# Kernel tuning notes

Hardware: AMD Instinct MI355X
Metric: run time of the kernel (lower is better)

The kernel has to match this reference:

```python
import jax, jax.numpy as jnp
import numpy as np

D = 1024      # d_model
HD = 128      # shared k/v head dim == attn_expert_dim
EA = 8        # attention experts
KA = 2        # attention top-k
EF = 16       # ffn experts
KF = 2        # ffn top-k
FH = 512      # ffn expert hidden dim
MAXP = 64     # max relative positions
B, S = 4, 1024
EPS = 1e-5


def setup_inputs() -> dict:
    key = jax.random.key(0)
    ks = jax.random.split(key, 12)
    r = lambda i, shape, scale=0.02: jax.random.normal(ks[i], shape, jnp.float32) * scale
    return {
        "src": jax.random.normal(ks[0], (B, S, D), jnp.float32),
        "ln1_w": jnp.ones((D,), jnp.float32), "ln1_b": jnp.zeros((D,), jnp.float32),
        "ln2_w": jnp.ones((D,), jnp.float32), "ln2_b": jnp.zeros((D,), jnp.float32),
        "attn_gate_w": r(1, (D, EA)),
        "q_w": r(2, (EA, D, HD)), "q_b": jnp.zeros((EA, HD), jnp.float32),
        "k_w": r(3, (D, HD)), "k_b": jnp.zeros((HD,), jnp.float32),
        "v_w": r(4, (D, HD)), "v_b": jnp.zeros((HD,), jnp.float32),
        "o_w": r(5, (EA, HD, D)), "o_b": jnp.zeros((EA, D), jnp.float32),
        "rel_table": r(6, (2 * MAXP + 1, HD)),
        "ff_gate_w": r(7, (D, EF)),
        "ff_w1": r(8, (EF, D, FH)), "ff_b1": jnp.zeros((EF, FH), jnp.float32),
        "ff_w2": r(9, (EF, FH, D)), "ff_b2": jnp.zeros((EF, D), jnp.float32),
    }


def _layer_norm(x, w, b):
    mu = x.mean(-1, keepdims=True)
    var = ((x - mu) ** 2).mean(-1, keepdims=True)
    return (x - mu) * jax.lax.rsqrt(var + EPS) * w + b


def _topk_gates(logits, k):
    # top-k over router logits, softmax over the selected k, scatter to dense [.., E]
    top_vals, top_idx = jax.lax.top_k(logits, k)
    g = jax.nn.softmax(top_vals, axis=-1)
    onehot = jax.nn.one_hot(top_idx, logits.shape[-1], dtype=logits.dtype)  # [...,k,E]
    return jnp.einsum('...k,...ke->...e', g, onehot)


def _moa(x, gate_w, q_w, q_b, k_w, k_b, v_w, v_b, o_w, o_b, rel_table):
    # Mixture-of-attention: per-expert q/out projections, shared k/v, Shaw rel-pos.
    S_ = x.shape[1]
    gates = _topk_gates(x @ gate_w, KA)                                  # [B,S,EA]
    q = (jnp.einsum('bsd,edh->bseh', x, q_w) + q_b) * (HD ** -0.5)       # [B,S,EA,HD]
    k = x @ k_w + k_b                                                    # [B,S,HD]
    v = x @ v_w + v_b
    scores = jnp.einsum('bqeh,bkh->beqk', q, k)                          # [B,EA,S,S]
    rel_s = jnp.einsum('bqeh,rh->beqr', q, rel_table)                    # [B,EA,S,R]
    pos = jnp.arange(S_)
    rel_idx = jnp.clip(pos[None, :] - pos[:, None], -MAXP, MAXP) + MAXP  # [S,S]
    scores = scores + jnp.take_along_axis(rel_s, rel_idx[None, None], axis=-1)
    p = jax.nn.softmax(scores, axis=-1)
    ctx = jnp.einsum('beqk,bkh->bqeh', p, v)                             # [B,S,EA,HD]
    out = jnp.einsum('bqeh,ehd,bqe->bqd', ctx, o_w, gates)
    return out + jnp.einsum('bqe,ed->bqd', gates, o_b)


def _moe_ffn(x, gate_w, w1, b1, w2, b2):
    gates = _topk_gates(x @ gate_w, KF)                                  # [B,S,EF]
    h = jax.nn.relu(jnp.einsum('bsd,edh->bseh', x, w1) + b1)             # [B,S,EF,FH]
    out = jnp.einsum('bseh,ehd,bse->bsd', h, w2, gates)
    return out + jnp.einsum('bse,ed->bsd', gates, b2)


def reference(src, ln1_w, ln1_b, ln2_w, ln2_b, attn_gate_w, q_w, q_b, k_w, k_b,
              v_w, v_b, o_w, o_b, rel_table, ff_gate_w, ff_w1, ff_b1, ff_w2, ff_b2):
    # pre-LN residual block around MoE attention
    res = src
    xn = _layer_norm(src, ln1_w, ln1_b)
    x = res + _moa(xn, attn_gate_w, q_w, q_b, k_w, k_b, v_w, v_b, o_w, o_b, rel_table)
    # pre-LN residual block around MoE FFN
    res = x
    xn = _layer_norm(x, ln2_w, ln2_b)
    return res + _moe_ffn(xn, ff_gate_w, ff_w1, ff_b1, ff_w2, ff_b2)
```

## Files before the change

kernel.cpp:

```cpp
#include <hip/hip_runtime.h>

#define D 1024
#define HD 128
#define EA 8
#define EF 16
#define FH 512
#define MAXPOS 64
#define RNUM 129
#define RSTRIDE 132
#define SEQ 1024
#define NTOK 4096
#define NPAIR (NTOK * 2)
#define NPAD 8320
#define LN_EPS 1e-5f
#define QSCALE 0.08838834764831845f
#define BSTR 32
#define PROW 2048
#define NSPL 2

typedef __attribute__((ext_vector_type(8))) short bf16x8;
typedef __attribute__((ext_vector_type(4))) float f32x4;
typedef __attribute__((ext_vector_type(8))) unsigned short u16x8;

__device__ inline ushort f2b(float f) {
    union { float f; unsigned u; } v; v.f = f;
    unsigned r = (v.u + 0x7fffu + ((v.u >> 16) & 1u)) >> 16;
    return (ushort)r;
}
__device__ inline float b2f(ushort u) {
    union { unsigned u; float f; } v; v.u = (unsigned)u << 16; return v.f;
}

__device__ __forceinline__ void gll(const void* g, void* l) {
    __builtin_amdgcn_global_load_lds((const __attribute__((address_space(1))) void*)g,
                                     (__attribute__((address_space(3))) void*)l, 16, 0, 0);
}
__device__ __forceinline__ void wait_vm0() { asm volatile("s_waitcnt vmcnt(0)" ::: "memory"); }
__device__ __forceinline__ void wait_vm3() { asm volatile("s_waitcnt vmcnt(3)" ::: "memory"); }
__device__ __forceinline__ void bar() { __builtin_amdgcn_s_barrier(); }

__device__ inline void mfma_step(const short* Asb, const short* Bsb,
                                 int wr, int wc, int m16, int q, f32x4 (&acc)[2][4]) {
    bf16x8 af[2], bfr[4];
#pragma unroll
    for (int i = 0; i < 2; i++) af[i] = *(const bf16x8*)&Asb[(wr + i * 16 + m16) * BSTR + q * 8];
#pragma unroll
    for (int j = 0; j < 4; j++) bfr[j] = *(const bf16x8*)&Bsb[(wc + j * 16 + m16) * BSTR + q * 8];
#pragma unroll
    for (int i = 0; i < 2; i++)
#pragma unroll
        for (int j = 0; j < 4; j++)
            acc[i][j] = __builtin_amdgcn_mfma_f32_16x16x32_bf16(af[i], bfr[j], acc[i][j], 0, 0, 0);
}

#define KLOOP(NK, AP, BP0, BP1, STRIDE)                                          \
    gll(AP, &As[0][w * 512]); gll(BP0, &Bs[0][w * 1024]); gll(BP1, &Bs[0][w * 1024 + 512]); \
    gll(AP + STRIDE, &As[1][w * 512]); gll(BP0 + STRIDE, &Bs[1][w * 1024]);      \
    gll(BP1 + STRIDE, &Bs[1][w * 1024 + 512]);                                   \
    {                                                                            \
        int cur = 0;                                                             \
        for (int k = 0; k < NK; k++) {                                           \
            if (k < NK - 1) wait_vm3(); else wait_vm0();                         \
            bar();                                                               \
            mfma_step(As[cur], Bs[cur], wr, wc, m16, q, acc);                    \
            if (k + 2 < NK) {                                                    \
                bar();                                                           \
                gll(AP + (k + 2) * STRIDE, &As[cur][w * 512]);                   \
                gll(BP0 + (k + 2) * STRIDE, &Bs[cur][w * 1024]);                 \
                gll(BP1 + (k + 2) * STRIDE, &Bs[cur][w * 1024 + 512]);           \
            }                                                                    \
            cur ^= 1;                                                            \
        }                                                                        \
    }

__global__ void ln_kernel(const float* __restrict__ x, const float* __restrict__ w,
                          const float* __restrict__ b, float* __restrict__ y,
                          ushort* __restrict__ yb) {
    int row = blockIdx.x;
    const float* xr = x + (size_t)row * D;
    float v[4];
    float s = 0.f, s2 = 0.f;
#pragma unroll
    for (int i = 0; i < 4; i++) {
        v[i] = xr[threadIdx.x + i * 256];
        s += v[i]; s2 += v[i] * v[i];
    }
#pragma unroll
    for (int off = 32; off; off >>= 1) { s += __shfl_down(s, off); s2 += __shfl_down(s2, off); }
    __shared__ float red0[4], red1[4];
    int wave = threadIdx.x >> 6, lane = threadIdx.x & 63;
    if (lane == 0) { red0[wave] = s; red1[wave] = s2; }
    __syncthreads();
    float ts = red0[0] + red0[1] + red0[2] + red0[3];
    float ts2 = red1[0] + red1[1] + red1[2] + red1[3];
    float mu = ts * (1.f / D);
    float var = ts2 * (1.f / D) - mu * mu;
    float inv = rsqrtf(var + LN_EPS);
#pragma unroll
    for (int i = 0; i < 4; i++) {
        int d = threadIdx.x + i * 256;
        float o = (v[i] - mu) * inv * w[d] + b[d];
        y[(size_t)row * D + d] = o;
        yb[(size_t)row * D + d] = f2b(o);
    }
}

template <int E>
__global__ void router_kernel(const float* __restrict__ xn, const float* __restrict__ gw,
                              int* __restrict__ idx, float* __restrict__ gate) {
    int t = blockIdx.x;
    int lane = threadIdx.x;
    float acc[E];
#pragma unroll
    for (int e = 0; e < E; e++) acc[e] = 0.f;
    const float* xr = xn + (size_t)t * D;
    for (int d = lane; d < D; d += 64) {
        float xv = xr[d];
#pragma unroll
        for (int e = 0; e < E; e++) acc[e] += xv * gw[d * E + e];
    }
#pragma unroll
    for (int e = 0; e < E; e++) {
#pragma unroll
        for (int off = 32; off; off >>= 1) acc[e] += __shfl_down(acc[e], off);
    }
    if (lane == 0) {
        float v0 = -1e30f, v1 = -1e30f;
        int i0 = 0, i1 = 0;
#pragma unroll
        for (int e = 0; e < E; e++) {
            float a = acc[e];
            if (a > v0) { v1 = v0; i1 = i0; v0 = a; i0 = e; }
            else if (a > v1) { v1 = a; i1 = e; }
        }
        float g0 = 1.f / (1.f + expf(v1 - v0));
        idx[t * 2] = i0; idx[t * 2 + 1] = i1;
        gate[t * 2] = g0; gate[t * 2 + 1] = 1.f - g0;
    }
}

__global__ void zero_meta(int* __restrict__ ameta, int* __restrict__ fmeta) {
    if (threadIdx.x < 105) ameta[threadIdx.x] = 0;
    if (threadIdx.x < 48) fmeta[threadIdx.x] = 0;
}

__global__ void abin_count(const int* __restrict__ aidx, int* __restrict__ meta) {
    int i = blockIdx.x * 256 + threadIdx.x;
    if (i < NPAIR) {
        int e = aidx[i];
        int b = (i >> 1) >> 10;
        atomicAdd(&meta[e * 4 + b], 1);
    }
}
__global__ void abin_scan(int* __restrict__ meta) {
    if (threadIdx.x == 0 && blockIdx.x == 0) {
        int s = 0;
        for (int bin = 0; bin < 32; bin++) {
            if ((bin & 3) == 0) meta[96 + (bin >> 2)] = s;
            meta[32 + bin] = s; meta[64 + bin] = s; s += meta[bin];
        }
        meta[96 + 8] = s;
    }
}
__global__ void abin_scatter(const int* __restrict__ aidx, int* __restrict__ meta,
                             int* __restrict__ list, int* __restrict__ inv) {
    int i = blockIdx.x * 256 + threadIdx.x;
    if (i < NPAIR) {
        int e = aidx[i];
        int b = (i >> 1) >> 10;
        int pos = atomicAdd(&meta[64 + e * 4 + b], 1);
        list[pos] = i;
        inv[i] = pos;
    }
}

__global__ void bin_count(const int* __restrict__ fidx, int* __restrict__ meta) {
    int i = blockIdx.x * 256 + threadIdx.x;
    if (i < NPAIR) atomicAdd(&meta[fidx[i]], 1);
}
__global__ void bin_scan(int* __restrict__ meta) {
    if (threadIdx.x == 0 && blockIdx.x == 0) {
        int s = 0;
        for (int e = 0; e < EF; e++) { meta[16 + e] = s; meta[32 + e] = s; s += meta[e]; }
    }
}
__global__ void bin_scatter(const int* __restrict__ fidx, int* __restrict__ meta,
                            int* __restrict__ list, int* __restrict__ inv) {
    int i = blockIdx.x * 256 + threadIdx.x;
    if (i < NPAIR) {
        int e = fidx[i];
        int pos = atomicAdd(&meta[32 + e], 1);
        list[pos] = i;
        inv[i] = pos;
    }
}

template <int R, int C>
__device__ __forceinline__ void convT_body(const float* __restrict__ src, ushort* __restrict__ dst) {
    int r0 = blockIdx.x * 32, c0 = blockIdx.y * 32;
    __shared__ float tile[32][33];
    int tx = threadIdx.x & 31, ty = threadIdx.x >> 5;
#pragma unroll
    for (int i = 0; i < 32; i += 8)
        tile[ty + i][tx] = src[(size_t)(r0 + ty + i) * C + c0 + tx];
    __syncthreads();
#pragma unroll
    for (int i = 0; i < 32; i += 8)
        dst[(size_t)(c0 + ty + i) * R + r0 + tx] = f2b(tile[tx][ty + i]);
}
template <int R, int C>
__global__ void convT_kernel(const float* __restrict__ in, ushort* __restrict__ out) {
    int e = blockIdx.z;
    convT_body<R, C>(in + (size_t)e * R * C, out + (size_t)e * C * R);
}
__global__ void convT_kv(const float* __restrict__ kw, const float* __restrict__ vw,
                         ushort* __restrict__ kwt, ushort* __restrict__ vwt) {
    if (blockIdx.z == 0) convT_body<1024, 128>(kw, kwt);
    else                 convT_body<1024, 128>(vw, vwt);
}

__global__ void conv_kernel(const float* __restrict__ in, ushort* __restrict__ out, int n) {
    int i = blockIdx.x * 256 + threadIdx.x;
    if (i < n) out[i] = f2b(in[i]);
}

__global__ __launch_bounds__(256) void kv_mfma(
    const ushort* __restrict__ xnb, const ushort* __restrict__ kwt,
    const ushort* __restrict__ vwt, float* __restrict__ kpart, float* __restrict__ vpart) {
    const ushort* W = blockIdx.z ? vwt : kwt;
    float* outp = blockIdx.z ? vpart : kpart;
    int m0 = blockIdx.x * 64;
    int s = blockIdx.y;
    int kbase = s * 512;
    __shared__ __align__(16) short As[2][64 * BSTR];
    __shared__ __align__(16) short Bs[2][128 * BSTR];
    int tid = threadIdx.x, w = tid >> 6, lane = tid & 63;
    int sr = lane >> 2, sc = (lane & 3) * 8;
    const ushort* ap = xnb + (size_t)(m0 + w * 16 + sr) * D + kbase + sc;
    const ushort* bp0 = W + (size_t)(w * 32 + sr) * D + kbase + sc;
    const ushort* bp1 = bp0 + (size_t)16 * D;
    int wr = (w >> 1) * 32, wc = (w & 1) * 64;
    int m16 = lane & 15, q = lane >> 4;
    f32x4 acc[2][4] = {};
    KLOOP(16, ap, bp0, bp1, 32)
#pragma unroll
    for (int i = 0; i < 2; i++)
#pragma unroll
        for (int r = 0; r < 4; r++) {
            int m = m0 + wr + i * 16 + q * 4 + r;
#pragma unroll
            for (int j = 0; j < 4; j++)
                outp[((size_t)s * NTOK + m) * HD + wc + j * 16 + m16] = acc[i][j][r];
        }
}

__global__ void kv_reduce(const float* __restrict__ kpart, const float* __restrict__ vpart,
                          const float* __restrict__ kb, const float* __restrict__ vb,
                          ushort* __restrict__ kb16, float* __restrict__ vbf) {
    int t = blockIdx.x, h = threadIdx.x;
    float ka = kb[h], va = vb[h];
#pragma unroll
    for (int s = 0; s < NSPL; s++) {
        ka += kpart[((size_t)s * NTOK + t) * HD + h];
        va += vpart[((size_t)s * NTOK + t) * HD + h];
    }
    kb16[(size_t)t * HD + h] = f2b(ka);
    vbf[(size_t)t * HD + h] = va;
}

__global__ __launch_bounds__(256) void q_mfma(
    const ushort* __restrict__ xnb, const ushort* __restrict__ qwt,
    const int* __restrict__ meta, const int* __restrict__ list, float* __restrict__ qpart) {
    int e = blockIdx.z;
    int o = meta[96 + e], c = meta[97 + e] - o;
    int m0 = blockIdx.x * 64;
    if (m0 >= c) return;
    int s = blockIdx.y;
    int kbase = s * 512;
    __shared__ __align__(16) short As[2][64 * BSTR];
    __shared__ __align__(16) short Bs[2][128 * BSTR];
    int tid = threadIdx.x, w = tid >> 6, lane = tid & 63;
    int sr = lane >> 2, sc = (lane & 3) * 8;
    int ri = o + m0 + w * 16 + sr; if (ri > NPAIR - 1) ri = NPAIR - 1;
    const ushort* ap = xnb + (size_t)(list[ri] >> 1) * D + kbase + sc;
    const ushort* bp0 = qwt + (size_t)e * HD * D + (size_t)(w * 32 + sr) * D + kbase + sc;
    const ushort* bp1 = bp0 + (size_t)16 * D;
    int wr = (w >> 1) * 32, wc = (w & 1) * 64;
    int m16 = lane & 15, q = lane >> 4;
    f32x4 acc[2][4] = {};
    KLOOP(16, ap, bp0, bp1, 32)
#pragma unroll
    for (int i = 0; i < 2; i++)
#pragma unroll
        for (int r = 0; r < 4; r++) {
            int pos = o + m0 + wr + i * 16 + q * 4 + r;
            if (pos < o + c) {
#pragma unroll
                for (int j = 0; j < 4; j++)
                    qpart[((size_t)s * NPAD + pos) * HD + wc + j * 16 + m16] = acc[i][j][r];
            }
        }
}

__global__ void q_reduce(const float* __restrict__ qpart, const float* __restrict__ qb,
                         const int* __restrict__ aidx, const int* __restrict__ list,
                         ushort* __restrict__ Qg) {
    int pos = blockIdx.x, h = threadIdx.x;
    int e = aidx[list[pos]];
    float a = qb[e * HD + h];
#pragma unroll
    for (int s = 0; s < NSPL; s++) a += qpart[((size_t)s * NPAD + pos) * HD + h];
    Qg[(size_t)pos * HD + h] = f2b(a * QSCALE);
}

__global__ __launch_bounds__(256) void rel_mfma(
    const ushort* __restrict__ Qg, const ushort* __restrict__ relb,
    float* __restrict__ R) {
    int m0 = blockIdx.x * 64;
    int n0 = blockIdx.y * 128;
    __shared__ __align__(16) short As[2][64 * BSTR];
    __shared__ __align__(16) short Bs[2][128 * BSTR];
    int tid = threadIdx.x, w = tid >> 6, lane = tid & 63;
    int sr = lane >> 2, sc = (lane & 3) * 8;
    const ushort* ap = Qg + (size_t)(m0 + w * 16 + sr) * HD + sc;
    int r0 = n0 + w * 32 + sr;      if (r0 > RNUM - 1) r0 = RNUM - 1;
    int r1 = n0 + w * 32 + 16 + sr; if (r1 > RNUM - 1) r1 = RNUM - 1;
    const ushort* bp0 = relb + (size_t)r0 * HD + sc;
    const ushort* bp1 = relb + (size_t)r1 * HD + sc;
    int wr = (w >> 1) * 32, wc = (w & 1) * 64;
    int m16 = lane & 15, q = lane >> 4;
    f32x4 acc[2][4] = {};
    KLOOP(4, ap, bp0, bp1, 32)
#pragma unroll
    for (int i = 0; i < 2; i++)
#pragma unroll
        for (int r = 0; r < 4; r++) {
            int pos = m0 + wr + i * 16 + q * 4 + r;
#pragma unroll
            for (int j = 0; j < 4; j++) {
                int n = n0 + wc + j * 16 + m16;
                if (n < RNUM) R[(size_t)pos * RSTRIDE + n] = acc[i][j][r];
            }
        }
}

__global__ __launch_bounds__(256) void s_mfma(
    const ushort* __restrict__ Qg, const ushort* __restrict__ kb16,
    const float* __restrict__ R, const int* __restrict__ meta,
    const int* __restrict__ list, float* __restrict__ S) {
    int bin = blockIdx.z;
    int o = meta[32 + bin], c = meta[bin];
    int m0 = blockIdx.x * 64;
    if (m0 >= c) return;
    int b = bin & 3;
    int n0 = blockIdx.y * 128;
    __shared__ __align__(16) short As[2][64 * BSTR];
    __shared__ __align__(16) short Bs[2][128 * BSTR];
    int tid = threadIdx.x, w = tid >> 6, lane = tid & 63;
    int sr = lane >> 2, sc = (lane & 3) * 8;
    int ar = o + m0 + w * 16 + sr; if (ar > NPAIR - 1) ar = NPAIR - 1;
    const ushort* ap = Qg + (size_t)ar * HD + sc;
    const ushort* bp0 = kb16 + ((size_t)b * SEQ + n0 + w * 32 + sr) * HD + sc;
    const ushort* bp1 = bp0 + (size_t)16 * HD;
    int wr = (w >> 1) * 32, wc = (w & 1) * 64;
    int m16 = lane & 15, q = lane >> 4;
    f32x4 acc[2][4] = {};
    KLOOP(4, ap, bp0, bp1, 32)
#pragma unroll
    for (int i = 0; i < 2; i++)
#pragma unroll
        for (int r = 0; r < 4; r++) {
            int pos = o + m0 + wr + i * 16 + q * 4 + r;
            if (pos < o + c) {
                int qpos = (list[pos] >> 1) & (SEQ - 1);
                const float* Rrow = R + (size_t)pos * RSTRIDE;
                float* sr_ = S + (size_t)pos * SEQ;
#pragma unroll
                for (int j = 0; j < 4; j++) {
                    int key = n0 + wc + j * 16 + m16;
                    int rix = key - qpos;
                    rix = (rix < -MAXPOS ? -MAXPOS : (rix > MAXPOS ? MAXPOS : rix)) + MAXPOS;
                    sr_[key] = acc[i][j][r] + Rrow[rix];
                }
            }
        }
}

__global__ __launch_bounds__(256) void softmax_kernel(float* __restrict__ S) {
    int row = blockIdx.x;
    float4* sr = (float4*)(S + (size_t)row * SEQ);
    float4 v = sr[threadIdx.x];
    float m = fmaxf(fmaxf(v.x, v.y), fmaxf(v.z, v.w));
#pragma unroll
    for (int off = 32; off; off >>= 1) m = fmaxf(m, __shfl_down(m, off));
    __shared__ float red0[4], red1[4];
    int wave = threadIdx.x >> 6, lane = threadIdx.x & 63;
    if (lane == 0) red0[wave] = m;
    __syncthreads();
    m = fmaxf(fmaxf(red0[0], red0[1]), fmaxf(red0[2], red0[3]));
    v.x = __expf(v.x - m); v.y = __expf(v.y - m);
    v.z = __expf(v.z - m); v.w = __expf(v.w - m);
    float s = v.x + v.y + v.z + v.w;
#pragma unroll
    for (int off = 32; off; off >>= 1) s += __shfl_down(s, off);
    if (lane == 0) red1[wave] = s;
    __syncthreads();
    float inv = 1.f / (red1[0] + red1[1] + red1[2] + red1[3]);
    ushort* pr = (ushort*)(S + (size_t)row * SEQ);
    ushort4 p4 = { f2b(v.x * inv), f2b(v.y * inv), f2b(v.z * inv), f2b(v.w * inv) };
    *(ushort4*)(pr + threadIdx.x * 4) = p4;
}

__global__ __launch_bounds__(256) void pv_mfma(
    const ushort* __restrict__ Pb, const ushort* __restrict__ vt16,
    const int* __restrict__ meta, float* __restrict__ ppart) {
    int bin = blockIdx.z;
    int o = meta[32 + bin], c = meta[bin];
    int m0 = blockIdx.x * 64;
    if (m0 >= c) return;
    int b = bin & 3;
    int s = blockIdx.y;
    int kbase = s * 512;
    __shared__ __align__(16) short As[2][64 * BSTR];
    __shared__ __align__(16) short Bs[2][128 * BSTR];
    int tid = threadIdx.x, w = tid >> 6, lane = tid & 63;
    int sr = lane >> 2, sc = (lane & 3) * 8;
    int ar = o + m0 + w * 16 + sr; if (ar > NPAIR - 1) ar = NPAIR - 1;
    const ushort* ap = Pb + (size_t)ar * PROW + kbase + sc;
    const ushort* bp0 = vt16 + (size_t)b * HD * SEQ + (size_t)(w * 32 + sr) * SEQ + kbase + sc;
    const ushort* bp1 = bp0 + (size_t)16 * SEQ;
    int wr = (w >> 1) * 32, wc = (w & 1) * 64;
    int m16 = lane & 15, q = lane >> 4;
    f32x4 acc[2][4] = {};
    KLOOP(16, ap, bp0, bp1, 32)
#pragma unroll
    for (int i = 0; i < 2; i++)
#pragma unroll
        for (int r = 0; r < 4; r++) {
            int pos = o + m0 + wr + i * 16 + q * 4 + r;
            if (pos < o + c) {
#pragma unroll
                for (int j = 0; j < 4; j++)
                    ppart[((size_t)s * NPAD + pos) * HD + wc + j * 16 + m16] = acc[i][j][r];
            }
        }
}

__global__ void pv_reduce(const float* __restrict__ ppart, const float* __restrict__ aga,
                          const int* __restrict__ list, ushort* __restrict__ ctx16) {
    int pos = blockIdx.x, h = threadIdx.x;
    float g = aga[list[pos]];
    float a = 0.f;
#pragma unroll
    for (int s = 0; s < NSPL; s++) a += ppart[((size_t)s * NPAD + pos) * HD + h];
    ctx16[(size_t)pos * HD + h] = f2b(a * g);
}

__global__ __launch_bounds__(256) void o_mfma(
    const ushort* __restrict__ ctx16, const ushort* __restrict__ owt,
    const int* __restrict__ meta, ushort* __restrict__ Ofb) {
    int e = blockIdx.z;
    int o = meta[96 + e], c = meta[97 + e] - o;
    int m0 = blockIdx.x * 64;
    if (m0 >= c) return;
    int n0 = blockIdx.y * 128;
    __shared__ __align__(16) short As[2][64 * BSTR];
    __shared__ __align__(16) short Bs[2][128 * BSTR];
    int tid = threadIdx.x, w = tid >> 6, lane = tid & 63;
    int sr = lane >> 2, sc = (lane & 3) * 8;
    int ar = o + m0 + w * 16 + sr; if (ar > NPAIR - 1) ar = NPAIR - 1;
    const ushort* ap = ctx16 + (size_t)ar * HD + sc;
    const ushort* bp0 = owt + (size_t)e * D * HD + (size_t)(n0 + w * 32 + sr) * HD + sc;
    const ushort* bp1 = bp0 + (size_t)16 * HD;
    int wr = (w >> 1) * 32, wc = (w & 1) * 64;
    int m16 = lane & 15, q = lane >> 4;
    f32x4 acc[2][4] = {};
    KLOOP(4, ap, bp0, bp1, 32)
#pragma unroll
    for (int i = 0; i < 2; i++)
#pragma unroll
        for (int r = 0; r < 4; r++) {
            int pos = o + m0 + wr + i * 16 + q * 4 + r;
            if (pos < o + c) {
#pragma unroll
                for (int j = 0; j < 4; j++)
                    Ofb[(size_t)pos * D + n0 + wc + j * 16 + m16] = f2b(acc[i][j][r]);
            }
        }
}

__global__ void attn_combine(const float* __restrict__ src, const float* __restrict__ ob,
                             const int* __restrict__ aidx, const float* __restrict__ aga,
                             const int* __restrict__ ainv, const ushort* __restrict__ Ofb,
                             float* __restrict__ x1) {
    int t = blockIdx.x, tid = threadIdx.x;
    int e0 = aidx[t * 2], e1 = aidx[t * 2 + 1];
    float g0 = aga[t * 2], g1 = aga[t * 2 + 1];
    int p0 = ainv[t * 2], p1 = ainv[t * 2 + 1];
#pragma unroll
    for (int i = 0; i < 4; i++) {
        int d = tid + i * 256;
        x1[(size_t)t * D + d] = src[(size_t)t * D + d]
                              + g0 * ob[e0 * D + d] + g1 * ob[e1 * D + d]
                              + b2f(Ofb[(size_t)p0 * D + d]) + b2f(Ofb[(size_t)p1 * D + d]);
    }
}

__global__ __launch_bounds__(256) void ffn_mfma1(
    const ushort* __restrict__ xnb2, const ushort* __restrict__ w1t,
    const float* __restrict__ b1, const int* __restrict__ meta,
    const int* __restrict__ list, const float* __restrict__ fga,
    ushort* __restrict__ Hb) {
    int e = blockIdx.z;
    int o = meta[16 + e], c = meta[e];
    int m0 = blockIdx.x * 64;
    if (m0 >= c) return;
    int n0 = blockIdx.y * 128;
    __shared__ __align__(16) short As[2][64 * BSTR];
    __shared__ __align__(16) short Bs[2][128 * BSTR];
    int tid = threadIdx.x, w = tid >> 6, lane = tid & 63;
    int sr = lane >> 2, sc = (lane & 3) * 8;
    int ri = o + m0 + w * 16 + sr; if (ri > NPAIR - 1) ri = NPAIR - 1;
    const ushort* ap = xnb2 + (size_t)(list[ri] >> 1) * D + sc;
    const ushort* bp0 = w1t + ((size_t)e * FH + n0 + w * 32 + sr) * D + sc;
    const ushort* bp1 = bp0 + (size_t)16 * D;
    int wr = (w >> 1) * 32, wc = (w & 1) * 64;
    int m16 = lane & 15, q = lane >> 4;
    f32x4 acc[2][4] = {};
    KLOOP(32, ap, bp0, bp1, 32)
#pragma unroll
    for (int i = 0; i < 2; i++)
#pragma unroll
        for (int r = 0; r < 4; r++) {
            int pos = o + m0 + wr + i * 16 + q * 4 + r;
            if (pos < o + c) {
                float g = fga[list[pos]];
#pragma unroll
                for (int j = 0; j < 4; j++) {
                    int n = n0 + wc + j * 16 + m16;
                    Hb[(size_t)pos * FH + n] = f2b(g * fmaxf(acc[i][j][r] + b1[e * FH + n], 0.f));
                }
            }
        }
}

__global__ __launch_bounds__(256) void ffn_mfma2(
    const ushort* __restrict__ Hb, const ushort* __restrict__ w2t,
    const int* __restrict__ meta, ushort* __restrict__ Of2b) {
    int e = blockIdx.z;
    int o = meta[16 + e], c = meta[e];
    int m0 = blockIdx.x * 64;
    if (m0 >= c) return;
    int n0 = blockIdx.y * 128;
    __shared__ __align__(16) short As[2][64 * BSTR];
    __shared__ __align__(16) short Bs[2][128 * BSTR];
    int tid = threadIdx.x, w = tid >> 6, lane = tid & 63;
    int sr = lane >> 2, sc = (lane & 3) * 8;
    int ar = o + m0 + w * 16 + sr; if (ar > NPAIR - 1) ar = NPAIR - 1;
    const ushort* ap = Hb + (size_t)ar * FH + sc;
    const ushort* bp0 = w2t + ((size_t)e * D + n0 + w * 32 + sr) * FH + sc;
    const ushort* bp1 = bp0 + (size_t)16 * FH;
    int wr = (w >> 1) * 32, wc = (w & 1) * 64;
    int m16 = lane & 15, q = lane >> 4;
    f32x4 acc[2][4] = {};
    KLOOP(16, ap, bp0, bp1, 32)
#pragma unroll
    for (int i = 0; i < 2; i++)
#pragma unroll
        for (int r = 0; r < 4; r++) {
            int pos = o + m0 + wr + i * 16 + q * 4 + r;
            if (pos < o + c) {
#pragma unroll
                for (int j = 0; j < 4; j++)
                    Of2b[(size_t)pos * D + n0 + wc + j * 16 + m16] = f2b(acc[i][j][r]);
            }
        }
}

__global__ void ffn_combine(const float* __restrict__ x1, const float* __restrict__ b2,
                            const int* __restrict__ fidx, const float* __restrict__ fga,
                            const int* __restrict__ finv, const ushort* __restrict__ Of2b,
                            float* __restrict__ out) {
    int t = blockIdx.x, tid = threadIdx.x;
    int e0 = fidx[t * 2], e1 = fidx[t * 2 + 1];
    float g0 = fga[t * 2], g1 = fga[t * 2 + 1];
    int p0 = finv[t * 2], p1 = finv[t * 2 + 1];
#pragma unroll
    for (int i = 0; i < 4; i++) {
        int d = tid + i * 256;
        out[(size_t)t * D + d] = x1[(size_t)t * D + d]
                               + g0 * b2[e0 * D + d] + g1 * b2[e1 * D + d]
                               + b2f(Of2b[(size_t)p0 * D + d]) + b2f(Of2b[(size_t)p1 * D + d]);
    }
}

extern "C" void kernel_launch(void* const* d_in, const int* in_sizes, int n_in,
                              void* d_out, int out_size, void* d_ws, size_t ws_size,
                              hipStream_t stream) {
    const float* src   = (const float*)d_in[0];
    const float* ln1_w = (const float*)d_in[1];
    const float* ln1_b = (const float*)d_in[2];
    const float* ln2_w = (const float*)d_in[3];
    const float* ln2_b = (const float*)d_in[4];
    const float* agw   = (const float*)d_in[5];
    const float* qw    = (const float*)d_in[6];
    const float* qb    = (const float*)d_in[7];
    const float* kw    = (const float*)d_in[8];
    const float* kb    = (const float*)d_in[9];
    const float* vw    = (const float*)d_in[10];
    const float* vb    = (const float*)d_in[11];
    const float* ow    = (const float*)d_in[12];
    const float* ob    = (const float*)d_in[13];
    const float* rel   = (const float*)d_in[14];
    const float* fgw   = (const float*)d_in[15];
    const float* w1    = (const float*)d_in[16];
    const float* b1    = (const float*)d_in[17];
    const float* w2    = (const float*)d_in[18];
    const float* b2    = (const float*)d_in[19];
    float* out = (float*)d_out;

    char* p = (char*)d_ws;
    float* xn1  = (float*)p; p += (size_t)NTOK * D * 4;
    float* x1   = (float*)p; p += (size_t)NTOK * D * 4;
    char*  sreg = p;         p += (size_t)NPAD * SEQ * 4;
    float*  Sbuf = (float*)sreg;
    ushort* Pb   = (ushort*)sreg;
    ushort* Ofb  = (ushort*)sreg;
    ushort* w1t  = (ushort*)sreg;
    ushort* w2t  = (ushort*)(sreg + (size_t)16777216);
    char*  reg  = p;         p += (size_t)NPAD * 128 * 6 + (size_t)NPAIR * RSTRIDE * 4;
    ushort* ctx16 = (ushort*)reg;
    ushort* Qg   = (ushort*)(reg + (size_t)NPAD * 128 * 4);
    float*  Rbuf = (float*)(reg + (size_t)NPAD * 128 * 6);
    ushort* Hb   = (ushort*)reg;
    char*  arena = p;        p += (size_t)4 * NPAD * 128 * 4;
    float*  kpart = (float*)arena;
    float*  vpart = (float*)(arena + (size_t)NSPL * NTOK * HD * 4);
    float*  qpart = (float*)arena;
    float*  ppart = (float*)arena;
    ushort* Of2b  = (ushort*)arena;
    ushort* kb16 = (ushort*)p; p += (size_t)NTOK * HD * 2;
    float* vbf  = (float*)p; p += (size_t)NTOK * HD * 4;
    ushort* vt16 = (ushort*)p; p += (size_t)NTOK * HD * 2;
    ushort* kwt = (ushort*)p; p += (size_t)HD * D * 2;
    ushort* vwt = (ushort*)p; p += (size_t)HD * D * 2;
    ushort* qwt = (ushort*)p; p += (size_t)EA * HD * D * 2;
    ushort* owt = (ushort*)p; p += (size_t)EA * D * HD * 2;
    ushort* relb = (ushort*)p; p += (size_t)RNUM * HD * 2 + 256;
    int*   aidx = (int*)p;   p += NPAIR * 4;
    float* aga  = (float*)p; p += NPAIR * 4;
    int*   fidx = (int*)p;   p += NPAIR * 4;
    float* fga  = (float*)p; p += NPAIR * 4;
    int*   ameta = (int*)p;  p += 128 * 4;
    int*   alist = (int*)p;  p += NPAIR * 4;
    int*   ainv = (int*)p;   p += NPAIR * 4;
    int*   fmeta = (int*)p;  p += 64 * 4;
    int*   flist = (int*)p;  p += NPAIR * 4;
    int*   finv = (int*)p;   p += NPAIR * 4;
    ushort* xnb = (ushort*)p; p += (size_t)NTOK * D * 2;
    float* xn2 = xn1;

    zero_meta<<<1, 128, 0, stream>>>(ameta, fmeta);
    ln_kernel<<<NTOK, 256, 0, stream>>>(src, ln1_w, ln1_b, xn1, xnb);
    router_kernel<EA><<<NTOK, 64, 0, stream>>>(xn1, agw, aidx, aga);
    abin_count<<<NPAIR / 256, 256, 0, stream>>>(aidx, ameta);
    abin_scan<<<1, 64, 0, stream>>>(ameta);
    abin_scatter<<<NPAIR / 256, 256, 0, stream>>>(aidx, ameta, alist, ainv);
    convT_kv<<<dim3(32, 4, 2), 256, 0, stream>>>(kw, vw, kwt, vwt);
    convT_kernel<1024, 128><<<dim3(32, 4, EA), 256, 0, stream>>>(qw, qwt);
    convT_kernel<128, 1024><<<dim3(4, 32, EA), 256, 0, stream>>>(ow, owt);
    conv_kernel<<<(RNUM * HD + 255) / 256, 256, 0, stream>>>(rel, relb, RNUM * HD);
    kv_mfma<<<dim3(64, NSPL, 2), 256, 0, stream>>>(xnb, kwt, vwt, kpart, vpart);
    kv_reduce<<<NTOK, 128, 0, stream>>>(kpart, vpart, kb, vb, kb16, vbf);
    convT_kernel<1024, 128><<<dim3(32, 4, 4), 256, 0, stream>>>(vbf, vt16);
    q_mfma<<<dim3(40, NSPL, EA), 256, 0, stream>>>(xnb, qwt, ameta, alist, qpart);
    q_reduce<<<NPAIR, 128, 0, stream>>>(qpart, qb, aidx, alist, Qg);
    rel_mfma<<<dim3(NPAIR / 64, 2), 256, 0, stream>>>(Qg, relb, Rbuf);
    s_mfma<<<dim3(12, 8, 32), 256, 0, stream>>>(Qg, kb16, Rbuf, ameta, alist, Sbuf);
    softmax_kernel<<<NPAIR, 256, 0, stream>>>(Sbuf);
    pv_mfma<<<dim3(12, NSPL, 32), 256, 0, stream>>>(Pb, vt16, ameta, ppart);
    pv_reduce<<<NPAIR, 128, 0, stream>>>(ppart, aga, alist, ctx16);
    o_mfma<<<dim3(40, 8, EA), 256, 0, stream>>>(ctx16, owt, ameta, Ofb);
    attn_combine<<<NTOK, 256, 0, stream>>>(src, ob, aidx, aga, ainv, Ofb, x1);

    ln_kernel<<<NTOK, 256, 0, stream>>>(x1, ln2_w, ln2_b, xn2, xnb);
    router_kernel<EF><<<NTOK, 64, 0, stream>>>(xn2, fgw, fidx, fga);
    bin_count<<<NPAIR / 256, 256, 0, stream>>>(fidx, fmeta);
    bin_scan<<<1, 64, 0, stream>>>(fmeta);
    bin_scatter<<<NPAIR / 256, 256, 0, stream>>>(fidx, fmeta, flist, finv);
    convT_kernel<1024, 512><<<dim3(32, 16, EF), 256, 0, stream>>>(w1, w1t);
    convT_kernel<512, 1024><<<dim3(16, 32, EF), 256, 0, stream>>>(w2, w2t);
    ffn_mfma1<<<dim3(20, 4, EF), 256, 0, stream>>>(xnb, w1t, b1, fmeta, flist, fga, Hb);
    ffn_mfma2<<<dim3(20, 8, EF), 256, 0, stream>>>(Hb, w2t, fmeta, Of2b);
    ffn_combine<<<NTOK, 256, 0, stream>>>(x1, b2, fidx, fga, finv, Of2b, out);
}
```

Baseline: 492.5 us.

## Fuse scores, softmax and PV into a single flash-attention kernel

Replaces the separate score GEMM, softmax, PV GEMM and split-K reduce kernels with one fused kernel that uses an online softmax. Each block holds 64 query rows and streams 128-key K/V tiles through swizzled LDS, adding the relative-position bias inline and writing bf16 probabilities back into the Q buffer for the PV MFMA. This removes the large fp32 score matrix round trip through global memory and three launches. In exchange there are fewer blocks (no key or split-K parallelism), extra barriers, and K/V loads are only partly overlapped with compute.

```diff
diff --git a/kernel.cpp b/kernel.cpp
--- a/kernel.cpp
+++ b/kernel.cpp
@@ -35,8 +35,10 @@
     __builtin_amdgcn_global_load_lds((const __attribute__((address_space(1))) void*)g,
                                      (__attribute__((address_space(3))) void*)l, 16, 0, 0);
 }
-__device__ __forceinline__ void wait_vm0() { asm volatile("s_waitcnt vmcnt(0)" ::: "memory"); }
-__device__ __forceinline__ void wait_vm3() { asm volatile("s_waitcnt vmcnt(3)" ::: "memory"); }
+__device__ __forceinline__ void wait_vm0()  { asm volatile("s_waitcnt vmcnt(0)" ::: "memory"); }
+__device__ __forceinline__ void wait_vm3()  { asm volatile("s_waitcnt vmcnt(3)" ::: "memory"); }
+__device__ __forceinline__ void wait_vm8()  { asm volatile("s_waitcnt vmcnt(8)" ::: "memory"); }
+__device__ __forceinline__ void wait_vm16() { asm volatile("s_waitcnt vmcnt(16)" ::: "memory"); }
 __device__ __forceinline__ void bar() { __builtin_amdgcn_s_barrier(); }
 
 __device__ inline void mfma_step(const short* Asb, const short* Bsb,
@@ -344,116 +346,161 @@
         }
 }
 
-__global__ __launch_bounds__(256) void s_mfma(
+__global__ __launch_bounds__(256) void flash_attn(
     const ushort* __restrict__ Qg, const ushort* __restrict__ kb16,
-    const float* __restrict__ R, const int* __restrict__ meta,
-    const int* __restrict__ list, float* __restrict__ S) {
+    const ushort* __restrict__ vt16, const float* __restrict__ Rbuf,
+    const int* __restrict__ meta, const int* __restrict__ list,
+    const float* __restrict__ aga, ushort* __restrict__ ctx16) {
     int bin = blockIdx.z;
     int o = meta[32 + bin], c = meta[bin];
     int m0 = blockIdx.x * 64;
     if (m0 >= c) return;
     int b = bin & 3;
-    int n0 = blockIdx.y * 128;
-    __shared__ __align__(16) short As[2][64 * BSTR];
-    __shared__ __align__(16) short Bs[2][128 * BSTR];
+    __shared__ __align__(16) ushort QP[64 * 128];
+    __shared__ __align__(16) ushort KV[2][128 * 128];
     int tid = threadIdx.x, w = tid >> 6, lane = tid & 63;
-    int sr = lane >> 2, sc = (lane & 3) * 8;
-    int ar = o + m0 + w * 16 + sr; if (ar > NPAIR - 1) ar = NPAIR - 1;
-    const ushort* ap = Qg + (size_t)ar * HD + sc;
-    const ushort* bp0 = kb16 + ((size_t)b * SEQ + n0 + w * 32 + sr) * HD + sc;
-    const ushort* bp1 = bp0 + (size_t)16 * HD;
-    int wr = (w >> 1) * 32, wc = (w & 1) * 64;
     int m16 = lane & 15, q = lane >> 4;
-    f32x4 acc[2][4] = {};
-    KLOOP(4, ap, bp0, bp1, 32)
-#pragma unroll
-    for (int i = 0; i < 2; i++)
+    int srow4 = lane >> 4, scol = lane & 15;
+
+#pragma unroll
+    for (int t = 0; t < 4; t++) {
+        int row = w * 16 + t * 4 + srow4;
+        int rg = o + m0 + row; if (rg > NPAIR - 1) rg = NPAIR - 1;
+        gll(Qg + (size_t)rg * HD + ((scol ^ (row & 7)) * 8), &QP[(w * 16 + t * 4) * 128]);
+    }
+#pragma unroll
+    for (int u = 0; u < 8; u++) {
+        int row = w * 32 + u * 4 + srow4;
+        gll(kb16 + ((size_t)b * SEQ + row) * HD + ((scol ^ (row & 7)) * 8), &KV[0][(w * 32 + u * 4) * 128]);
+    }
+#pragma unroll
+    for (int u = 0; u < 8; u++) {
+        int row = w * 32 + u * 4 + srow4;
+        gll(vt16 + ((size_t)b * HD + row) * SEQ + ((scol ^ (row & 7)) * 8), &KV[1][(w * 32 + u * 4) * 128]);
+    }
+
+    int lid[4]; int qpos[4]; const float* Rrow[4];
+#pragma unroll
+    for (int r = 0; r < 4; r++) {
+        int pos = o + m0 + w * 16 + q * 4 + r;
+        int pc = pos < NPAIR ? pos : NPAIR - 1;
+        lid[r] = list[pc];
+        qpos[r] = (lid[r] >> 1) & (SEQ - 1);
+        Rrow[r] = Rbuf + (size_t)pc * RSTRIDE;
+    }
+    float m_run[4], l_run[4];
+#pragma unroll
+    for (int r = 0; r < 4; r++) { m_run[r] = -1e30f; l_run[r] = 0.f; }
+    f32x4 acc_o[8];
+#pragma unroll
+    for (int j = 0; j < 8; j++) acc_o[j] = (f32x4){0.f, 0.f, 0.f, 0.f};
+
+    wait_vm16();
+    bf16x8 qf[4];
+#pragma unroll
+    for (int kk = 0; kk < 4; kk++)
+        qf[kk] = *(const bf16x8*)&QP[(w * 16 + m16) * 128 + (((q + 4 * kk) ^ (m16 & 7)) * 8)];
+
+    for (int kt = 0; kt < 8; kt++) {
+        wait_vm8();
+        bar();
+        f32x4 s_[8];
+#pragma unroll
+        for (int j = 0; j < 8; j++) s_[j] = (f32x4){0.f, 0.f, 0.f, 0.f};
+#pragma unroll
+        for (int kk = 0; kk < 4; kk++) {
+#pragma unroll
+            for (int j = 0; j < 8; j++) {
+                bf16x8 bb = *(const bf16x8*)&KV[0][(j * 16 + m16) * 128 + (((q + 4 * kk) ^ (m16 & 7)) * 8)];
+                s_[j] = __builtin_amdgcn_mfma_f32_16x16x32_bf16(qf[kk], bb, s_[j], 0, 0, 0);
+            }
+        }
+        float mloc[4] = {-1e30f, -1e30f, -1e30f, -1e30f};
+#pragma unroll
+        for (int j = 0; j < 8; j++) {
+            int key = kt * 128 + j * 16 + m16;
+#pragma unroll
+            for (int r = 0; r < 4; r++) {
+                int rix = key - qpos[r];
+                rix = (rix < -MAXPOS ? -MAXPOS : (rix > MAXPOS ? MAXPOS : rix)) + MAXPOS;
+                float vv = s_[j][r] + Rrow[r][rix];
+                s_[j][r] = vv;
+                mloc[r] = fmaxf(mloc[r], vv);
+            }
+        }
+#pragma unroll
+        for (int off = 8; off; off >>= 1)
+#pragma unroll
+            for (int r = 0; r < 4; r++) mloc[r] = fmaxf(mloc[r], __shfl_xor(mloc[r], off, 16));
+        float scale_[4], lloc[4] = {0.f, 0.f, 0.f, 0.f};
 #pragma unroll
         for (int r = 0; r < 4; r++) {
-            int pos = o + m0 + wr + i * 16 + q * 4 + r;
-            if (pos < o + c) {
-                int qpos = (list[pos] >> 1) & (SEQ - 1);
-                const float* Rrow = R + (size_t)pos * RSTRIDE;
-                float* sr_ = S + (size_t)pos * SEQ;
-#pragma unroll
-                for (int j = 0; j < 4; j++) {
-                    int key = n0 + wc + j * 16 + m16;
-                    int rix = key - qpos;
-                    rix = (rix < -MAXPOS ? -MAXPOS : (rix > MAXPOS ? MAXPOS : rix)) + MAXPOS;
-                    sr_[key] = acc[i][j][r] + Rrow[rix];
-                }
-            }
-        }
-}
-
-__global__ __launch_bounds__(256) void softmax_kernel(float* __restrict__ S) {
-    int row = blockIdx.x;
-    float4* sr = (float4*)(S + (size_t)row * SEQ);
-    float4 v = sr[threadIdx.x];
-    float m = fmaxf(fmaxf(v.x, v.y), fmaxf(v.z, v.w));
-#pragma unroll
-    for (int off = 32; off; off >>= 1) m = fmaxf(m, __shfl_down(m, off));
-    __shared__ float red0[4], red1[4];
-    int wave = threadIdx.x >> 6, lane = threadIdx.x & 63;
-    if (lane == 0) red0[wave] = m;
-    __syncthreads();
-    m = fmaxf(fmaxf(red0[0], red0[1]), fmaxf(red0[2], red0[3]));
-    v.x = __expf(v.x - m); v.y = __expf(v.y - m);
-    v.z = __expf(v.z - m); v.w = __expf(v.w - m);
-    float s = v.x + v.y + v.z + v.w;
-#pragma unroll
-    for (int off = 32; off; off >>= 1) s += __shfl_down(s, off);
-    if (lane == 0) red1[wave] = s;
-    __syncthreads();
-    float inv = 1.f / (red1[0] + red1[1] + red1[2] + red1[3]);
-    ushort* pr = (ushort*)(S + (size_t)row * SEQ);
-    ushort4 p4 = { f2b(v.x * inv), f2b(v.y * inv), f2b(v.z * inv), f2b(v.w * inv) };
-    *(ushort4*)(pr + threadIdx.x * 4) = p4;
-}
-
-__global__ __launch_bounds__(256) void pv_mfma(
-    const ushort* __restrict__ Pb, const ushort* __restrict__ vt16,
-    const int* __restrict__ meta, float* __restrict__ ppart) {
-    int bin = blockIdx.z;
-    int o = meta[32 + bin], c = meta[bin];
-    int m0 = blockIdx.x * 64;
-    if (m0 >= c) return;
-    int b = bin & 3;
-    int s = blockIdx.y;
-    int kbase = s * 512;
-    __shared__ __align__(16) short As[2][64 * BSTR];
-    __shared__ __align__(16) short Bs[2][128 * BSTR];
-    int tid = threadIdx.x, w = tid >> 6, lane = tid & 63;
-    int sr = lane >> 2, sc = (lane & 3) * 8;
-    int ar = o + m0 + w * 16 + sr; if (ar > NPAIR - 1) ar = NPAIR - 1;
-    const ushort* ap = Pb + (size_t)ar * PROW + kbase + sc;
-    const ushort* bp0 = vt16 + (size_t)b * HD * SEQ + (size_t)(w * 32 + sr) * SEQ + kbase + sc;
-    const ushort* bp1 = bp0 + (size_t)16 * SEQ;
-    int wr = (w >> 1) * 32, wc = (w & 1) * 64;
-    int m16 = lane & 15, q = lane >> 4;
-    f32x4 acc[2][4] = {};
-    KLOOP(16, ap, bp0, bp1, 32)
-#pragma unroll
-    for (int i = 0; i < 2; i++)
-#pragma unroll
-        for (int r = 0; r < 4; r++) {
-            int pos = o + m0 + wr + i * 16 + q * 4 + r;
-            if (pos < o + c) {
-#pragma unroll
-                for (int j = 0; j < 4; j++)
-                    ppart[((size_t)s * NPAD + pos) * HD + wc + j * 16 + m16] = acc[i][j][r];
-            }
-        }
-}
-
-__global__ void pv_reduce(const float* __restrict__ ppart, const float* __restrict__ aga,
-                          const int* __restrict__ list, ushort* __restrict__ ctx16) {
-    int pos = blockIdx.x, h = threadIdx.x;
-    float g = aga[list[pos]];
-    float a = 0.f;
-#pragma unroll
-    for (int s = 0; s < NSPL; s++) a += ppart[((size_t)s * NPAD + pos) * HD + h];
-    ctx16[(size_t)pos * HD + h] = f2b(a * g);
+            float mn = fmaxf(m_run[r], mloc[r]);
+            scale_[r] = __expf(m_run[r] - mn);
+            m_run[r] = mn;
+        }
+#pragma unroll
+        for (int j = 0; j < 8; j++) {
+#pragma unroll
+            for (int r = 0; r < 4; r++) {
+                float p = __expf(s_[j][r] - m_run[r]);
+                lloc[r] += p;
+                int row = q * 4 + r;
+                QP[(w * 16 + row) * 128 + ((j * 16 + m16) ^ ((row & 7) * 8))] = f2b(p);
+            }
+        }
+#pragma unroll
+        for (int off = 8; off; off >>= 1)
+#pragma unroll
+            for (int r = 0; r < 4; r++) lloc[r] += __shfl_xor(lloc[r], off, 16);
+#pragma unroll
+        for (int r = 0; r < 4; r++) l_run[r] = l_run[r] * scale_[r] + lloc[r];
+#pragma unroll
+        for (int j = 0; j < 8; j++)
+#pragma unroll
+            for (int r = 0; r < 4; r++) acc_o[j][r] *= scale_[r];
+        bar();
+        if (kt < 7) {
+#pragma unroll
+            for (int u = 0; u < 8; u++) {
+                int row = w * 32 + u * 4 + srow4;
+                gll(kb16 + ((size_t)b * SEQ + (kt + 1) * 128 + row) * HD + ((scol ^ (row & 7)) * 8),
+                    &KV[0][(w * 32 + u * 4) * 128]);
+            }
+            wait_vm8();
+        } else {
+            wait_vm0();
+        }
+        bar();
+#pragma unroll
+        for (int kk = 0; kk < 4; kk++) {
+            bf16x8 pf = *(const bf16x8*)&QP[(w * 16 + m16) * 128 + (((q + 4 * kk) ^ (m16 & 7)) * 8)];
+#pragma unroll
+            for (int j = 0; j < 8; j++) {
+                bf16x8 vv = *(const bf16x8*)&KV[1][(j * 16 + m16) * 128 + (((q + 4 * kk) ^ (m16 & 7)) * 8)];
+                acc_o[j] = __builtin_amdgcn_mfma_f32_16x16x32_bf16(pf, vv, acc_o[j], 0, 0, 0);
+            }
+        }
+        bar();
+        if (kt < 7) {
+#pragma unroll
+            for (int u = 0; u < 8; u++) {
+                int row = w * 32 + u * 4 + srow4;
+                gll(vt16 + ((size_t)b * HD + row) * SEQ + (kt + 1) * 128 + ((scol ^ (row & 7)) * 8),
+                    &KV[1][(w * 32 + u * 4) * 128]);
+            }
+        }
+    }
+#pragma unroll
+    for (int r = 0; r < 4; r++) {
+        int pos = o + m0 + w * 16 + q * 4 + r;
+        if (pos < o + c) {
+            float g = aga[lid[r]] / l_run[r];
+#pragma unroll
+            for (int j = 0; j < 8; j++)
+                ctx16[(size_t)pos * HD + j * 16 + m16] = f2b(acc_o[j][r] * g);
+        }
+    }
 }
 
 __global__ __launch_bounds__(256) void o_mfma(
@@ -623,8 +670,6 @@
     float* xn1  = (float*)p; p += (size_t)NTOK * D * 4;
     float* x1   = (float*)p; p += (size_t)NTOK * D * 4;
     char*  sreg = p;         p += (size_t)NPAD * SEQ * 4;
-    float*  Sbuf = (float*)sreg;
-    ushort* Pb   = (ushort*)sreg;
     ushort* Ofb  = (ushort*)sreg;
     ushort* w1t  = (ushort*)sreg;
     ushort* w2t  = (ushort*)(sreg + (size_t)16777216);
@@ -637,7 +682,6 @@
     float*  kpart = (float*)arena;
     float*  vpart = (float*)(arena + (size_t)NSPL * NTOK * HD * 4);
     float*  qpart = (float*)arena;
-    float*  ppart = (float*)arena;
     ushort* Of2b  = (ushort*)arena;
     ushort* kb16 = (ushort*)p; p += (size_t)NTOK * HD * 2;
     float* vbf  = (float*)p; p += (size_t)NTOK * HD * 4;
@@ -676,10 +720,7 @@
     q_mfma<<<dim3(40, NSPL, EA), 256, 0, stream>>>(xnb, qwt, ameta, alist, qpart);
     q_reduce<<<NPAIR, 128, 0, stream>>>(qpart, qb, aidx, alist, Qg);
     rel_mfma<<<dim3(NPAIR / 64, 2), 256, 0, stream>>>(Qg, relb, Rbuf);
-    s_mfma<<<dim3(12, 8, 32), 256, 0, stream>>>(Qg, kb16, Rbuf, ameta, alist, Sbuf);
-    softmax_kernel<<<NPAIR, 256, 0, stream>>>(Sbuf);
-    pv_mfma<<<dim3(12, NSPL, 32), 256, 0, stream>>>(Pb, vt16, ameta, ppart);
-    pv_reduce<<<NPAIR, 128, 0, stream>>>(ppart, aga, alist, ctx16);
+    flash_attn<<<dim3(12, 1, 32), 256, 0, stream>>>(Qg, kb16, vt16, Rbuf, ameta, alist, aga, ctx16);
     o_mfma<<<dim3(40, 8, EA), 256, 0, stream>>>(ctx16, owt, ameta, Ofb);
     attn_combine<<<NTOK, 256, 0, stream>>>(src, ob, aidx, aga, ainv, Ofb, x1);
 
```

New measurement: 516.7 us. 1.05x slower.
